# Optimization experiments

Measured on AMD Instinct MI355X. Metric: run time of the kernel, lower is better.

The kernel has to match this reference:

```python
import jax, jax.numpy as jnp
import numpy as np

N_NODES = 50000
N_PAIRS = 400000
F_IN = 5
GCN_DIMS = [32, 64, 128]
MLP_DIMS = [128, 64]


def _lin_init(key, out_d, in_d):
    return jax.random.normal(key, (out_d, in_d), dtype=jnp.float32) / np.sqrt(in_d)


def setup_inputs() -> dict:
    rng = np.random.default_rng(0)
    hi = rng.integers(1, N_NODES, size=N_PAIRS)
    lo = rng.integers(0, 2**31 - 1, size=N_PAIRS) % hi  # lo < hi strictly
    # each undirected pair appears twice per direction (two parallel edges / classes)
    src = np.concatenate([hi, hi, lo, lo]).astype(np.int32)
    dst = np.concatenate([lo, lo, hi, hi]).astype(np.int32)
    edges = jnp.asarray(np.stack([src, dst]))  # [2, 4P]
    detector_labels = jnp.asarray(rng.random(N_NODES) < 0.9)
    key = jax.random.key(0)
    ks = jax.random.split(key, 16)
    x = jax.random.normal(ks[0], (N_NODES, F_IN), dtype=jnp.float32)
    edge_attr = jax.random.uniform(ks[1], (4 * N_PAIRS, 2), dtype=jnp.float32)
    inp = {"x": x, "edges": edges, "edge_attr": edge_attr, "detector_labels": detector_labels}
    dims = [F_IN] + GCN_DIMS
    for i, (di, do) in enumerate(zip(dims[:-1], dims[1:])):
        inp[f"gc{i}_Wrel"] = _lin_init(ks[2 + 3 * i], do, di)
        inp[f"gc{i}_brel"] = jnp.zeros((do,), dtype=jnp.float32)
        inp[f"gc{i}_Wroot"] = _lin_init(ks[3 + 3 * i], do, di)
    mdims = [2 * GCN_DIMS[-1] + 1] + MLP_DIMS
    for i, (di, do) in enumerate(zip(mdims[:-1], mdims[1:])):
        inp[f"fc{i}_W"] = _lin_init(ks[11 + 2 * i], do, di)
        inp[f"fc{i}_b"] = jnp.zeros((do,), dtype=jnp.float32)
    inp["out_W"] = _lin_init(ks[15], 1, MLP_DIMS[-1])
    inp["out_b"] = jnp.zeros((1,), dtype=jnp.float32)
    return inp


def _edge_perm(edges_np, det_np):
    # SplitSyndromes: keep edges with both endpoints in detector set, src > dst,
    # then sort_edge_index (stable lexicographic sort by (src, dst)).
    src, dst = edges_np[0], edges_np[1]
    valid = det_np[src] & det_np[dst] & (src > dst)
    idx = np.where(valid)[0]
    order = np.lexsort((dst[idx], src[idx]))
    return idx[order]


def reference(x, edges, edge_attr, detector_labels,
              gc0_Wrel, gc0_brel, gc0_Wroot,
              gc1_Wrel, gc1_brel, gc1_Wroot,
              gc2_Wrel, gc2_brel, gc2_Wroot,
              fc0_W, fc0_b, fc1_W, fc1_b, out_W, out_b):
    src, dst = edges[0], edges[1]
    w = edge_attr[:, 0] * edge_attr[:, 1]  # GraphConv edge weight
    # GraphConv: lin_rel(sum_j w_ji * x_j) + lin_root(x), ReLU
    for Wrel, brel, Wroot in ((gc0_Wrel, gc0_brel, gc0_Wroot),
                              (gc1_Wrel, gc1_brel, gc1_Wroot),
                              (gc2_Wrel, gc2_brel, gc2_Wroot)):
        agg = jax.ops.segment_sum(x[src] * w[:, None], dst, num_segments=N_NODES)
        x = jax.nn.relu(agg @ Wrel.T + brel + x @ Wroot.T)
    perm = _edge_perm(np.asarray(edges), np.asarray(detector_labels))
    e_src = edges[0, perm]
    e_dst = edges[1, perm]
    ea = edge_attr[perm]  # [M, 2]
    feat = jnp.concatenate([x[e_src], ea[:, :1], x[e_dst]], axis=-1)  # [M, 257]
    for W, b in ((fc0_W, fc0_b), (fc1_W, fc1_b)):
        feat = jax.nn.relu(feat @ W.T + b)
    score = feat @ out_W.T + out_b  # [M, 1]
    pair = jnp.concatenate([score[::2], score[1::2]], axis=1)  # [M/2, 2]
    cls = jnp.stack([ea[::2, 1], ea[1::2, 1]], axis=1)  # [M/2, 2]
    mi = jnp.argmin(pair, axis=1)
    sel = jnp.take_along_axis(pair, mi[:, None], axis=1)[:, 0]
    cls_sel = jnp.take_along_axis(cls, mi[:, None], axis=1)[:, 0]
    edges_out = jnp.stack([e_src[::2], e_dst[::2]])
    return edges_out, jax.nn.sigmoid(sel), cls_sel
```

## Files before the change

kernel.cpp:

```cpp
#include <hip/hip_runtime.h>
#include <hip/hip_bf16.h>
#include <stdint.h>

typedef unsigned long long ull;
typedef unsigned short us;
typedef __attribute__((ext_vector_type(8))) short short8;
typedef __attribute__((ext_vector_type(4))) float f32x4;
#define IDX_BITS 22
#define IDX_MASK 0x3FFFFFu

__device__ __forceinline__ float bfq(float x) {
    return __bfloat162float(__float2bfloat16(x));
}
__device__ __forceinline__ us bfu(float x) {
    __hip_bfloat16 b = __float2bfloat16(x);
    return *(us*)&b;
}
__device__ __forceinline__ float b2f(us u) {
    return __bfloat162float(*(__hip_bfloat16*)&u);
}
__device__ __forceinline__ float ldx(const float* p, size_t i) { return p[i]; }
__device__ __forceinline__ float ldx(const us* p, size_t i) { return b2f(p[i]); }


__global__ void k_det8(const int* __restrict__ src, const int* __restrict__ dst,
                       const unsigned char* __restrict__ det, int P, int* __restrict__ stats,
                       int* __restrict__ dcnt, int* __restrict__ scnt,
                       int2* __restrict__ rnk, int* __restrict__ vrnk) {
    __shared__ int blkc;
    if (threadIdx.x == 0) blkc = 0;
    __syncthreads();
    int e = blockIdx.x * blockDim.x + threadIdx.x;
    bool v = false;
    if (e < P) {
        int hi = src[e], lo = dst[e];
        int r1 = atomicAdd(&dcnt[lo], 1);
        int r2 = atomicAdd(&dcnt[hi], 1);
        rnk[e] = make_int2(r1, r2);
        v = (det[hi] != 0) && (det[lo] != 0);
        vrnk[e] = v ? atomicAdd(&scnt[hi], 1) : -1;
    }
    ull b = __ballot(v);
    if ((threadIdx.x & 63) == 0 && b) atomicAdd(&blkc, (int)__popcll(b));
    __syncthreads();
    if (threadIdx.x == 0 && blkc) atomicAdd(&stats[0], blkc);
}
__global__ void k_det16(const int* __restrict__ src, const int* __restrict__ dst,
                        const us* __restrict__ det, int P, int* __restrict__ stats) {
    if (stats[3] != -1) return;
    __shared__ int blkc;
    if (threadIdx.x == 0) blkc = 0;
    __syncthreads();
    int e = blockIdx.x * blockDim.x + threadIdx.x;
    bool v = false;
    if (e < P) v = (det[src[e]] != 0) && (det[dst[e]] != 0);
    ull b = __ballot(v);
    if ((threadIdx.x & 63) == 0 && b) atomicAdd(&blkc, (int)__popcll(b));
    __syncthreads();
    if (threadIdx.x == 0 && blkc) atomicAdd(&stats[1], blkc);
}
__global__ void k_det32(const int* __restrict__ src, const int* __restrict__ dst,
                        const unsigned int* __restrict__ det, int P, int* __restrict__ stats) {
    if (stats[3] != -2) return;
    __shared__ int blkc;
    if (threadIdx.x == 0) blkc = 0;
    __syncthreads();
    int e = blockIdx.x * blockDim.x + threadIdx.x;
    bool v = false;
    if (e < P) v = (det[src[e]] != 0) && (det[dst[e]] != 0);
    ull b = __ballot(v);
    if ((threadIdx.x & 63) == 0 && b) atomicAdd(&blkc, (int)__popcll(b));
    __syncthreads();
    if (threadIdx.x == 0 && blkc) atomicAdd(&stats[2], blkc);
}
__global__ void k_mode(int* stats, int osz, int step) {
    if (step == 1) {
        int c = stats[0];
        stats[3] = (c == osz / 4 || c == osz / 2) ? 0 : -1;
    } else if (step == 2) {
        if (stats[3] == -1) {
            int c = stats[1];
            stats[3] = (c == osz / 4 || c == osz / 2) ? 2 : -2;
        }
    } else {
        if (stats[3] == -2) stats[3] = 1;
        int m = stats[3];
        stats[4] = (m == 0) ? stats[0] : (m == 2) ? stats[1] : stats[2];
    }
}
__device__ __forceinline__ bool det_ok(int n, const void* det, int mode) {
    if (mode == 0) return ((const unsigned char*)det)[n] != 0;
    if (mode == 2) return ((const us*)det)[n] != 0;
    return ((const unsigned int*)det)[n] != 0;
}

__global__ void k_fixzero(const int* __restrict__ stats, int* __restrict__ scnt, int N) {
    if (stats[3] == 0) return;
    int i = blockIdx.x * blockDim.x + threadIdx.x;
    if (i < N) scnt[i] = 0;
}
__global__ void k_fixhist(const int* __restrict__ src, const int* __restrict__ dst,
                          const void* __restrict__ det, const int* __restrict__ stats,
                          int* __restrict__ scnt, int* __restrict__ vrnk, int P) {
    int m = stats[3];
    if (m == 0) return;
    int e = blockIdx.x * blockDim.x + threadIdx.x;
    if (e >= P) return;
    int hi = src[e], lo = dst[e];
    bool v = det_ok(hi, det, m) && det_ok(lo, det, m);
    vrnk[e] = v ? atomicAdd(&scnt[hi], 1) : -1;
}

__global__ __launch_bounds__(1024) void k_scanA(const int* __restrict__ cnt,
                                                int* __restrict__ off,
                                                int* __restrict__ bsum, int n) {
    __shared__ int wsum[16];
    int t = threadIdx.x, lane = t & 63, w = t >> 6;
    int i = blockIdx.x * 1024 + t;
    int v = (i < n) ? cnt[i] : 0;
    int inc = v;
#pragma unroll
    for (int s = 1; s < 64; s <<= 1) {
        int u = __shfl_up(inc, s);
        if (lane >= s) inc += u;
    }
    if (lane == 63) wsum[w] = inc;
    __syncthreads();
    if (t < 16) {
        int x = wsum[t], sc = x;
#pragma unroll
        for (int s = 1; s < 16; s <<= 1) {
            int u = __shfl_up(sc, s);
            if (t >= s) sc += u;
        }
        wsum[t] = sc - x;
    }
    __syncthreads();
    if (i < n) off[i] = wsum[w] + inc - v;
    if (t == 1023) bsum[blockIdx.x] = wsum[15] + inc;
}
__global__ void k_scanB(int* __restrict__ bsum, int* __restrict__ off, int nb, int n) {
    int t = threadIdx.x;
    int v = (t < nb) ? bsum[t] : 0;
    int inc = v;
#pragma unroll
    for (int s = 1; s < 64; s <<= 1) {
        int u = __shfl_up(inc, s);
        if (t >= s) inc += u;
    }
    if (t < nb) bsum[t] = inc - v;
    if (t == 63) off[n] = inc;
}
__global__ __launch_bounds__(1024) void k_scanC(int* __restrict__ off,
                                                const int* __restrict__ bsum, int n) {
    int i = blockIdx.x * 1024 + threadIdx.x;
    if (i < n && blockIdx.x > 0) off[i] += bsum[blockIdx.x];
}

__global__ void k_scatter(const int* __restrict__ src, const int* __restrict__ dst,
                          const float* __restrict__ ea, const int* __restrict__ doff,
                          const int2* __restrict__ rnk, int2* __restrict__ epair, int P) {
    int e = blockIdx.x * blockDim.x + threadIdx.x;
    if (e >= P) return;
    int hi = src[e], lo = dst[e];
    float w1 = ea[2 * e] * ea[2 * e + 1] + ea[2 * (e + P)] * ea[2 * (e + P) + 1];
    float w2 = ea[2 * (2 * P + e)] * ea[2 * (2 * P + e) + 1] +
               ea[2 * (3 * P + e)] * ea[2 * (3 * P + e) + 1];
    int2 r = rnk[e];
    epair[doff[lo] + r.x] = make_int2(hi, __float_as_int(w1));
    epair[doff[hi] + r.y] = make_int2(lo, __float_as_int(w2));
}

__global__ void k_packall(const float* __restrict__ W1rel, const float* __restrict__ W1root,
                          const float* __restrict__ W2rel, const float* __restrict__ W2root,
                          const float* __restrict__ W3rel, const float* __restrict__ W3root,
                          const float* __restrict__ W0, const float* __restrict__ Wfc1,
                          us* __restrict__ pb1, us* __restrict__ pb2, us* __restrict__ pb3,
                          us* __restrict__ pbP, us* __restrict__ pbQ, us* __restrict__ w1f) {
    int gid = blockIdx.x * blockDim.x + threadIdx.x;
    const float* Wrel;
    const float* Wroot;
    us* out;
    int idx, FIN, CT;
    if (gid < 1024) { idx = gid; Wrel = W1rel; Wroot = W1root; out = pb1; FIN = 5; CT = 2; }
    else if (gid < 5120) { idx = gid - 1024; Wrel = W2rel; Wroot = W2root; out = pb2; FIN = 32; CT = 4; }
    else if (gid < 21504) { idx = gid - 5120; Wrel = W3rel; Wroot = W3root; out = pb3; FIN = 64; CT = 8; }
    else if (gid < 54272) {
        int i2 = gid - 21504;
        bool isQ = i2 >= 16384;
        int i = i2 & 16383;
        int j = i & 7, l = (i >> 3) & 63, ct = (i >> 9) & 7, ks = i >> 12;
        int k = ks * 32 + ((l >> 4) << 3) + j;
        int col = ct * 16 + (l & 15);
        float v = isQ ? W0[col * 257 + 129 + k] : W0[col * 257 + k];
        (isQ ? pbQ : pbP)[i] = bfu(v);
        return;
    } else if (gid < 62464) {
        int i = gid - 54272;
        int j = i & 7, l = (i >> 3) & 63, ct = (i >> 9) & 3, ks = i >> 11;
        int k = ks * 32 + ((l >> 4) << 3) + j;
        int col = ct * 16 + (l & 15);
        w1f[i] = bfu(Wfc1[col * 128 + k]);
        return;
    } else return;
    int j = idx & 7, l = (idx >> 3) & 63;
    int t = idx >> 9;
    int ct = t % CT, ks = t / CT;
    int k = ks * 32 + ((l >> 4) << 3) + j;
    int col = ct * 16 + (l & 15);
    float v = 0.f;
    if (k < FIN) v = Wrel[col * FIN + k];
    else if (k < 2 * FIN) v = Wroot[col * FIN + (k - FIN)];
    out[idx] = bfu(v);
}

template <int FIN, int KP, int G, typename TIN>
__global__ __launch_bounds__(256) void k_agg(
    const TIN* __restrict__ xin, const int2* __restrict__ epair,
    const int* __restrict__ doff, us* __restrict__ A, int N) {
    int tid = blockIdx.x * 256 + threadIdx.x;
    int n = tid / G, f = tid % G;
    if (n >= N) return;
    us* row = &A[(size_t)n * KP];
    if (f < FIN) {
        int b = doff[n], e2 = doff[n + 1];
        float a = 0.f;
        int j = b;
        for (; j + 8 <= e2; j += 8) {
            int2 pp[8];
#pragma unroll
            for (int u = 0; u < 8; ++u) pp[u] = epair[j + u];
            float xv[8];
#pragma unroll
            for (int u = 0; u < 8; ++u) xv[u] = ldx(xin, (size_t)pp[u].x * FIN + f);
#pragma unroll
            for (int u = 0; u < 8; ++u) a = fmaf(__int_as_float(pp[u].y), xv[u], a);
        }
        for (; j < e2; ++j) {
            int2 pq = epair[j];
            a = fmaf(__int_as_float(pq.y), ldx(xin, (size_t)pq.x * FIN + f), a);
        }
        row[f] = bfu(a);
        row[FIN + f] = bfu(ldx(xin, (size_t)n * FIN + f));
    }
    for (int c = 2 * FIN + f; c < KP; c += G) row[c] = 0;
}

template <int KP, int FOUT>
__global__ __launch_bounds__(256) void k_mm(
    const us* __restrict__ A, const us* __restrict__ bfrag,
    const float* __restrict__ bias, us* __restrict__ xout, int N) {
    constexpr int CT = FOUT / 16, KS = KP / 32, STR = KP + 8, CPR = KP / 8;
    __shared__ us Al[64 * STR];
    int t = threadIdx.x, lane = t & 63, w = t >> 6;
    int n0 = blockIdx.x * 64;
    for (int idx = t; idx < 64 * CPR; idx += 256) {
        int r = idx / CPR, c = idx % CPR;
        int n = n0 + r;
        uint4 v = (n < N) ? *(const uint4*)&A[(size_t)n * KP + c * 8] : make_uint4(0, 0, 0, 0);
        *(uint4*)&Al[r * STR + c * 8] = v;
    }
    __syncthreads();
    f32x4 acc[CT];
#pragma unroll
    for (int ct = 0; ct < CT; ++ct) acc[ct] = (f32x4){0.f, 0.f, 0.f, 0.f};
    int arow = w * 16 + (lane & 15);
    int koff = (lane >> 4) << 3;
#pragma unroll
    for (int ks = 0; ks < KS; ++ks) {
        short8 a = *(const short8*)&Al[arow * STR + ks * 32 + koff];
#pragma unroll
        for (int ct = 0; ct < CT; ++ct) {
            short8 b = ((const short8*)bfrag)[(ks * CT + ct) * 64 + lane];
            acc[ct] = __builtin_amdgcn_mfma_f32_16x16x32_bf16(a, b, acc[ct], 0, 0, 0);
        }
    }
    int g = lane >> 4, c0 = lane & 15;
#pragma unroll
    for (int ct = 0; ct < CT; ++ct) {
        int col = ct * 16 + c0;
        float bb = bias[col];
#pragma unroll
        for (int r2 = 0; r2 < 4; ++r2) {
            int n = n0 + w * 16 + g * 4 + r2;
            if (n < N) xout[(size_t)n * FOUT + col] = bfu(fmaxf(acc[ct][r2] + bb, 0.f));
        }
    }
}

__global__ __launch_bounds__(256) void k_mmPQ(
    const us* __restrict__ x3b, const us* __restrict__ pbP, const us* __restrict__ pbQ,
    const float* __restrict__ b0, us* __restrict__ P, us* __restrict__ Q, int N) {
    constexpr int CT = 8, KS = 4, STR = 136, CPR = 16;
    __shared__ us Al[64 * STR];
    int t = threadIdx.x, lane = t & 63, w = t >> 6;
    int n0 = blockIdx.x * 64;
    for (int idx = t; idx < 64 * CPR; idx += 256) {
        int r = idx / CPR, c = idx % CPR;
        int n = n0 + r;
        uint4 v = (n < N) ? *(const uint4*)&x3b[(size_t)n * 128 + c * 8] : make_uint4(0, 0, 0, 0);
        *(uint4*)&Al[r * STR + c * 8] = v;
    }
    __syncthreads();
    int arow = w * 16 + (lane & 15);
    int koff = (lane >> 4) << 3;
    int g = lane >> 4, c0 = lane & 15;
    f32x4 acc[CT];
#pragma unroll
    for (int ct = 0; ct < CT; ++ct) acc[ct] = (f32x4){0.f, 0.f, 0.f, 0.f};
#pragma unroll
    for (int ks = 0; ks < KS; ++ks) {
        short8 a = *(const short8*)&Al[arow * STR + ks * 32 + koff];
#pragma unroll
        for (int ct = 0; ct < CT; ++ct) {
            short8 b = ((const short8*)pbP)[(ks * CT + ct) * 64 + lane];
            acc[ct] = __builtin_amdgcn_mfma_f32_16x16x32_bf16(a, b, acc[ct], 0, 0, 0);
        }
    }
#pragma unroll
    for (int ct = 0; ct < CT; ++ct) {
        int col = ct * 16 + c0;
        float bb = b0[col];
#pragma unroll
        for (int r2 = 0; r2 < 4; ++r2) {
            int n = n0 + w * 16 + g * 4 + r2;
            if (n < N) P[(size_t)n * 128 + col] = bfu(acc[ct][r2] + bb);
        }
    }
#pragma unroll
    for (int ct = 0; ct < CT; ++ct) acc[ct] = (f32x4){0.f, 0.f, 0.f, 0.f};
#pragma unroll
    for (int ks = 0; ks < KS; ++ks) {
        short8 a = *(const short8*)&Al[arow * STR + ks * 32 + koff];
#pragma unroll
        for (int ct = 0; ct < CT; ++ct) {
            short8 b = ((const short8*)pbQ)[(ks * CT + ct) * 64 + lane];
            acc[ct] = __builtin_amdgcn_mfma_f32_16x16x32_bf16(a, b, acc[ct], 0, 0, 0);
        }
    }
#pragma unroll
    for (int ct = 0; ct < CT; ++ct) {
        int col = ct * 16 + c0;
#pragma unroll
        for (int r2 = 0; r2 < 4; ++r2) {
            int n = n0 + w * 16 + g * 4 + r2;
            if (n < N) Q[(size_t)n * 128 + col] = bfu(acc[ct][r2]);
        }
    }
}

__global__ void k_scatter_ent(const int* __restrict__ src, const int* __restrict__ dst,
                              const int* __restrict__ vrnk, const int* __restrict__ soff,
                              ull* __restrict__ ent, int P, int Mcap) {
    int e = blockIdx.x * blockDim.x + threadIdx.x;
    if (e >= P) return;
    int rv = vrnk[e];
    if (rv < 0) return;
    int hi = src[e], lo = dst[e];
    int p = soff[hi] + rv;
    if (p < Mcap) ent[p] = ((ull)(unsigned)lo << IDX_BITS) | (unsigned)e;
}

__global__ __launch_bounds__(256) void k_wsort(const int* __restrict__ off,
                                               ull* __restrict__ ent, int N, int Mcap) {
    int node = blockIdx.x * 4 + (threadIdx.x >> 6);
    int lane = threadIdx.x & 63;
    if (node >= N) return;
    int b = off[node], e2 = off[node + 1];
    if (e2 > Mcap) e2 = Mcap;
    int len = e2 - b;
    if (len <= 1) return;
    if (len <= 64) {
        ull key = (lane < len) ? ent[b + lane] : ~0ull;
        int phases = len + (len & 1);
        for (int ph = 0; ph < phases; ++ph) {
            int partner;
            if ((ph & 1) == 0) partner = lane ^ 1;
            else partner = (lane == 0 || lane == 63) ? lane
                                                     : ((lane & 1) ? lane + 1 : lane - 1);
            ull other = __shfl(key, partner);
            if (partner > lane) key = key < other ? key : other;
            else if (partner < lane) key = key > other ? key : other;
        }
        if (lane < len) ent[b + lane] = key;
    } else if (lane == 0) {
        for (int i = b + 1; i < e2; ++i) {
            ull k = ent[i];
            int j = i - 1;
            while (j >= b && ent[j] > k) { ent[j + 1] = ent[j]; --j; }
            ent[j + 1] = k;
        }
    }
}

__global__ __launch_bounds__(256) void k_mlp2(
    const us* __restrict__ Pm, const us* __restrict__ Qm, const float* __restrict__ ea,
    const int* __restrict__ src, const ull* __restrict__ ent, const int* __restrict__ stats,
    const float* __restrict__ W0, const us* __restrict__ w1f,
    const float* __restrict__ b1, const float* __restrict__ w2, const float* __restrict__ b2,
    float* __restrict__ out, int P) {
    int Mh = stats[4];
    int rows = 2 * Mh;
    int m0 = blockIdx.x * 64;
    if (m0 >= rows) return;
    __shared__ us A[64 * 136];
    __shared__ float ws0e[128];
    __shared__ int pHi[32], pLo[32];
    __shared__ float clsA[32], clsB[32];
    int t = threadIdx.x, lane = t & 63, w = t >> 6;
    if (t < 128) ws0e[t] = W0[t * 257 + 128];
    __syncthreads();

    {
        int j = t >> 3, q = t & 7;
        int pr = (m0 >> 1) + j;
        if (pr < Mh) {
            ull en = ent[pr];
            int e = (int)(en & IDX_MASK);
            int lo = (int)(en >> IDX_BITS);
            int hi = src[e];
            float eaA = ea[2 * e];
            float eaB = ea[2 * (e + P)];
            if (q == 0) {
                pHi[j] = hi;
                pLo[j] = lo;
                clsA[j] = ea[2 * e + 1];
                clsB[j] = ea[2 * (e + P) + 1];
            }
            const us* Pr = Pm + (size_t)hi * 128 + q * 16;
            const us* Qr = Qm + (size_t)lo * 128 + q * 16;
#pragma unroll
            for (int h = 0; h < 2; ++h) {
                int cb = q * 16 + h * 8;
                short8 pv = *(const short8*)&Pr[h * 8];
                short8 qv = *(const short8*)&Qr[h * 8];
                short8 ra, rb;
#pragma unroll
                for (int i = 0; i < 8; ++i) {
                    float base = b2f((us)pv[i]) + b2f((us)qv[i]);
                    float we = ws0e[cb + i];
                    ra[i] = (short)bfu(fmaxf(base + eaA * we, 0.f));
                    rb[i] = (short)bfu(fmaxf(base + eaB * we, 0.f));
                }
                *(short8*)&A[(2 * j) * 136 + cb] = ra;
                *(short8*)&A[(2 * j + 1) * 136 + cb] = rb;
            }
        } else {
            uint4 z = make_uint4(0, 0, 0, 0);
            *(uint4*)&A[(2 * j) * 136 + q * 16] = z;
            *(uint4*)&A[(2 * j) * 136 + q * 16 + 8] = z;
            *(uint4*)&A[(2 * j + 1) * 136 + q * 16] = z;
            *(uint4*)&A[(2 * j + 1) * 136 + q * 16 + 8] = z;
        }
    }
    __syncthreads();

    f32x4 acc1[4];
#pragma unroll
    for (int ct = 0; ct < 4; ++ct) acc1[ct] = (f32x4){0.f, 0.f, 0.f, 0.f};
    {
        int arow = w * 16 + (lane & 15);
        int koff = (lane >> 4) << 3;
#pragma unroll
        for (int ks = 0; ks < 4; ++ks) {
            short8 a = *(const short8*)&A[arow * 136 + ks * 32 + koff];
#pragma unroll
            for (int ct = 0; ct < 4; ++ct) {
                short8 b = ((const short8*)w1f)[(ks * 4 + ct) * 64 + lane];
                acc1[ct] = __builtin_amdgcn_mfma_f32_16x16x32_bf16(a, b, acc1[ct], 0, 0, 0);
            }
        }
    }
    {
        int g = lane >> 4, c0 = lane & 15;
        float part[4] = {0.f, 0.f, 0.f, 0.f};
#pragma unroll
        for (int ct = 0; ct < 4; ++ct) {
            int col = ct * 16 + c0;
            float bb = b1[col], wv = w2[col];
#pragma unroll
            for (int r = 0; r < 4; ++r)
                part[r] += fmaxf(acc1[ct][r] + bb, 0.f) * wv;
        }
        float bout = b2[0];
        float sv[4];
#pragma unroll
        for (int r = 0; r < 4; ++r) {
            float v = part[r];
            v += __shfl_xor(v, 1);
            v += __shfl_xor(v, 2);
            v += __shfl_xor(v, 4);
            v += __shfl_xor(v, 8);
            sv[r] = v + bout;
        }
        if (c0 == 0) {
#pragma unroll
            for (int rr = 0; rr < 4; rr += 2) {
                int jloc = (w * 16 + g * 4 + rr) >> 1;
                int pgi = (m0 >> 1) + jloc;
                if (pgi < Mh) {
                    float s0 = sv[rr], s1 = sv[rr + 1];
                    int pick = (s1 < s0) ? 1 : 0;
                    float sel = pick ? s1 : s0;
                    float cls = pick ? clsB[jloc] : clsA[jloc];
                    float sig = 1.f / (1.f + expf(-sel));
                    out[pgi] = bfq((float)pHi[jloc]);
                    out[Mh + pgi] = bfq((float)pLo[jloc]);
                    out[2 * Mh + pgi] = bfq(sig);
                    out[3 * Mh + pgi] = bfq(cls);
                }
            }
        }
    }
}

extern "C" void kernel_launch(void* const* d_in, const int* in_sizes, int n_in,
                              void* d_out, int out_size, void* d_ws, size_t ws_size,
                              hipStream_t stream) {
    const float* x0 = (const float*)d_in[0];
    const int* edges = (const int*)d_in[1];
    const float* ea = (const float*)d_in[2];
    const void* det = d_in[3];

    int N = in_sizes[0] / 5;
    int E = in_sizes[1] / 2;
    int P = E / 4;
    int osz = out_size;
    int Mcap = osz;

    const int* src = edges;
    const int* dst = edges + E;

    char* p = (char*)d_ws;
    auto alloc = [&](size_t bytes) {
        char* r = p;
        p += (bytes + 255) & ~(size_t)255;
        return r;
    };
    us* xa = (us*)alloc((size_t)N * 32 * 2);
    us* xb = (us*)alloc((size_t)N * 64 * 2);
    us* x3b = (us*)alloc((size_t)N * 128 * 2);
    us* Abuf = (us*)alloc((size_t)N * 128 * 2);
    us* Pb = Abuf;
    us* Qb = (us*)alloc((size_t)N * 128 * 2);
    us* pb1 = (us*)alloc(1024 * 2);
    us* pb2 = (us*)alloc(4096 * 2);
    us* pb3 = (us*)alloc(16384 * 2);
    us* pbP = (us*)alloc(16384 * 2);
    us* pbQ = (us*)alloc(16384 * 2);
    us* w1f = (us*)alloc(8192 * 2);
    int* bsum = (int*)alloc(256);
    int2* rnk = (int2*)alloc((size_t)P * 8);
    int* vrnk = (int*)alloc((size_t)P * 4);
    char* z0 = p;
    int* stats = (int*)alloc(256);
    int* dcnt = (int*)alloc((size_t)N * 4);
    int* scnt = (int*)alloc((size_t)N * 4);
    size_t zlen = (size_t)(p - z0);
    char* u0 = p;
    int* doff = (int*)alloc((size_t)(N + 1) * 4);
    int2* epair = (int2*)alloc((size_t)(2 * P) * 8);
    char* endB = p;
    p = u0;
    int* soff = (int*)alloc((size_t)(N + 1) * 4);
    ull* ent = (ull*)alloc((size_t)Mcap * 8);
    char* endC = p;
    size_t need = (size_t)(((endB > endC) ? endB : endC) - (char*)d_ws);
    if (need > ws_size) return;

    const int B = 256;
    int gP = (P + B - 1) / B;
    int nb = (N + 1023) / 1024;

    hipMemsetAsync(z0, 0, zlen, stream);

    k_det8<<<gP, B, 0, stream>>>(src, dst, (const unsigned char*)det, P, stats,
                                 dcnt, scnt, rnk, vrnk);
    k_mode<<<1, 1, 0, stream>>>(stats, osz, 1);
    k_det16<<<gP, B, 0, stream>>>(src, dst, (const us*)det, P, stats);
    k_mode<<<1, 1, 0, stream>>>(stats, osz, 2);
    k_det32<<<gP, B, 0, stream>>>(src, dst, (const unsigned int*)det, P, stats);
    k_mode<<<1, 1, 0, stream>>>(stats, osz, 3);
    k_fixzero<<<(N + B - 1) / B, B, 0, stream>>>(stats, scnt, N);
    k_fixhist<<<gP, B, 0, stream>>>(src, dst, det, stats, scnt, vrnk, P);

    k_packall<<<(62464 + B - 1) / B, B, 0, stream>>>(
        (const float*)d_in[4], (const float*)d_in[6],
        (const float*)d_in[7], (const float*)d_in[9],
        (const float*)d_in[10], (const float*)d_in[12],
        (const float*)d_in[13], (const float*)d_in[15],
        pb1, pb2, pb3, pbP, pbQ, w1f);

    k_scanA<<<nb, 1024, 0, stream>>>(dcnt, doff, bsum, N);
    k_scanB<<<1, 64, 0, stream>>>(bsum, doff, nb, N);
    k_scanC<<<nb, 1024, 0, stream>>>(doff, bsum, N);

    k_scatter<<<gP, B, 0, stream>>>(src, dst, ea, doff, rnk, epair, P);

    k_agg<5, 32, 8, float><<<((size_t)N * 8 + B - 1) / B, B, 0, stream>>>(
        x0, epair, doff, Abuf, N);
    k_mm<32, 32><<<(N + 63) / 64, B, 0, stream>>>(Abuf, pb1, (const float*)d_in[5], xa, N);
    k_agg<32, 64, 32, us><<<((size_t)N * 32 + B - 1) / B, B, 0, stream>>>(
        xa, epair, doff, Abuf, N);
    k_mm<64, 64><<<(N + 63) / 64, B, 0, stream>>>(Abuf, pb2, (const float*)d_in[8], xb, N);
    k_agg<64, 128, 64, us><<<((size_t)N * 64 + B - 1) / B, B, 0, stream>>>(
        xb, epair, doff, Abuf, N);
    k_mm<128, 128><<<(N + 63) / 64, B, 0, stream>>>(Abuf, pb3, (const float*)d_in[11], x3b, N);

    k_mmPQ<<<(N + 63) / 64, B, 0, stream>>>(x3b, pbP, pbQ, (const float*)d_in[14], Pb, Qb, N);

    k_scanA<<<nb, 1024, 0, stream>>>(scnt, soff, bsum, N);
    k_scanB<<<1, 64, 0, stream>>>(bsum, soff, nb, N);
    k_scanC<<<nb, 1024, 0, stream>>>(soff, bsum, N);
    k_scatter_ent<<<gP, B, 0, stream>>>(src, dst, vrnk, soff, ent, P, Mcap);
    k_wsort<<<(N + 3) / 4, B, 0, stream>>>(soff, ent, N, Mcap);

    k_mlp2<<<(osz + 63) / 64, B, 0, stream>>>(
        Pb, Qb, ea, src, ent, stats,
        (const float*)d_in[13], w1f,
        (const float*)d_in[16], (const float*)d_in[17], (const float*)d_in[18],
        (float*)d_out, P);
}
```

Before: 333.0 us.

## Store intermediate activations in FP8, fuse weight packing, merge scans and scatters

```diff
diff --git a/kernel.cpp b/kernel.cpp
--- a/kernel.cpp
+++ b/kernel.cpp
@@ -4,6 +4,7 @@
 
 typedef unsigned long long ull;
 typedef unsigned short us;
+typedef unsigned char u8;
 typedef __attribute__((ext_vector_type(8))) short short8;
 typedef __attribute__((ext_vector_type(4))) float f32x4;
 #define IDX_BITS 22
@@ -19,14 +20,89 @@
 __device__ __forceinline__ float b2f(us u) {
     return __bfloat162float(*(__hip_bfloat16*)&u);
 }
+__device__ __forceinline__ u8 f2q(float x) {
+    x = fminf(fmaxf(x, -448.f), 448.f);
+    unsigned int u = __float_as_uint(x);
+    unsigned int s = (u >> 24) & 0x80;
+    float ax = fabsf(x);
+    if (ax < 0.0009765625f) return (u8)s;
+    unsigned int au = u & 0x7FFFFFFF;
+    int e = (int)(au >> 23) - 127;
+    unsigned int m = au & 0x7FFFFF;
+    int E = e + 7;
+    if (E <= 0) {
+        int q = (int)rintf(ax * 512.f);
+        if (q >= 8) return (u8)(s | 0x08);
+        return (u8)(s | q);
+    }
+    unsigned int keep = m >> 20;
+    unsigned int rest = m & 0xFFFFF;
+    keep += (rest > 0x80000u || (rest == 0x80000u && (keep & 1)));
+    if (keep == 8) { keep = 0; ++E; }
+    if (E >= 16) return (u8)(s | 0x7E);
+    return (u8)(s | (E << 3) | keep);
+}
+__device__ __forceinline__ float q2f(u8 v) {
+    int E = (v >> 3) & 0xF, m = v & 7;
+    float mag = (E == 0) ? (float)m * 0.001953125f
+                         : __uint_as_float((unsigned)(((E + 120) << 23) | (m << 20)));
+    return (v & 0x80) ? -mag : mag;
+}
 __device__ __forceinline__ float ldx(const float* p, size_t i) { return p[i]; }
 __device__ __forceinline__ float ldx(const us* p, size_t i) { return b2f(p[i]); }
+__device__ __forceinline__ float ldx(const u8* p, size_t i) { return q2f(p[i]); }
+__device__ __forceinline__ void sto(us* p, size_t i, float v) { p[i] = bfu(v); }
+__device__ __forceinline__ void sto(u8* p, size_t i, float v) { p[i] = f2q(v); }
 
 
 __global__ void k_det8(const int* __restrict__ src, const int* __restrict__ dst,
-                       const unsigned char* __restrict__ det, int P, int* __restrict__ stats,
+                       const u8* __restrict__ det, int P, int gP, int* __restrict__ stats,
                        int* __restrict__ dcnt, int* __restrict__ scnt,
-                       int2* __restrict__ rnk, int* __restrict__ vrnk) {
+                       int2* __restrict__ rnk, int* __restrict__ vrnk,
+                       const float* __restrict__ W1rel, const float* __restrict__ W1root,
+                       const float* __restrict__ W2rel, const float* __restrict__ W2root,
+                       const float* __restrict__ W3rel, const float* __restrict__ W3root,
+                       const float* __restrict__ W0, const float* __restrict__ Wfc1,
+                       us* __restrict__ pb1, us* __restrict__ pb2, us* __restrict__ pb3,
+                       us* __restrict__ pbP, us* __restrict__ pbQ, us* __restrict__ w1f) {
+    if ((int)blockIdx.x >= gP) {
+        int gid = (blockIdx.x - gP) * 256 + threadIdx.x;
+        const float* Wrel;
+        const float* Wroot;
+        us* out;
+        int idx, FIN, CT;
+        if (gid < 1024) { idx = gid; Wrel = W1rel; Wroot = W1root; out = pb1; FIN = 5; CT = 2; }
+        else if (gid < 5120) { idx = gid - 1024; Wrel = W2rel; Wroot = W2root; out = pb2; FIN = 32; CT = 4; }
+        else if (gid < 21504) { idx = gid - 5120; Wrel = W3rel; Wroot = W3root; out = pb3; FIN = 64; CT = 8; }
+        else if (gid < 54272) {
+            int i2 = gid - 21504;
+            bool isQ = i2 >= 16384;
+            int i = i2 & 16383;
+            int j = i & 7, l = (i >> 3) & 63, ct = (i >> 9) & 7, ks = i >> 12;
+            int k = ks * 32 + ((l >> 4) << 3) + j;
+            int col = ct * 16 + (l & 15);
+            float v = isQ ? W0[col * 257 + 129 + k] : W0[col * 257 + k];
+            (isQ ? pbQ : pbP)[i] = bfu(v);
+            return;
+        } else if (gid < 62464) {
+            int i = gid - 54272;
+            int j = i & 7, l = (i >> 3) & 63, ct = (i >> 9) & 3, ks = i >> 11;
+            int k = ks * 32 + ((l >> 4) << 3) + j;
+            int col = ct * 16 + (l & 15);
+            w1f[i] = bfu(Wfc1[col * 128 + k]);
+            return;
+        } else return;
+        int j = idx & 7, l = (idx >> 3) & 63;
+        int t = idx >> 9;
+        int ct = t % CT, ks = t / CT;
+        int k = ks * 32 + ((l >> 4) << 3) + j;
+        int col = ct * 16 + (l & 15);
+        float v = 0.f;
+        if (k < FIN) v = Wrel[col * FIN + k];
+        else if (k < 2 * FIN) v = Wroot[col * FIN + (k - FIN)];
+        out[idx] = bfu(v);
+        return;
+    }
     __shared__ int blkc;
     if (threadIdx.x == 0) blkc = 0;
     __syncthreads();
@@ -89,11 +165,10 @@
     }
 }
 __device__ __forceinline__ bool det_ok(int n, const void* det, int mode) {
-    if (mode == 0) return ((const unsigned char*)det)[n] != 0;
+    if (mode == 0) return ((const u8*)det)[n] != 0;
     if (mode == 2) return ((const us*)det)[n] != 0;
     return ((const unsigned int*)det)[n] != 0;
 }
-
 __global__ void k_fixzero(const int* __restrict__ stats, int* __restrict__ scnt, int N) {
     if (stats[3] == 0) return;
     int i = blockIdx.x * blockDim.x + threadIdx.x;
@@ -139,17 +214,31 @@
     if (i < n) off[i] = wsum[w] + inc - v;
     if (t == 1023) bsum[blockIdx.x] = wsum[15] + inc;
 }
-__global__ void k_scanB(int* __restrict__ bsum, int* __restrict__ off, int nb, int n) {
-    int t = threadIdx.x;
+__global__ __launch_bounds__(1024) void k_scanB(int* __restrict__ bsum,
+                                                int* __restrict__ off, int nb, int n) {
+    __shared__ int wsum[16];
+    int t = threadIdx.x, lane = t & 63, w = t >> 6;
     int v = (t < nb) ? bsum[t] : 0;
     int inc = v;
 #pragma unroll
     for (int s = 1; s < 64; s <<= 1) {
         int u = __shfl_up(inc, s);
-        if (t >= s) inc += u;
-    }
-    if (t < nb) bsum[t] = inc - v;
-    if (t == 63) off[n] = inc;
+        if (lane >= s) inc += u;
+    }
+    if (lane == 63) wsum[w] = inc;
+    __syncthreads();
+    if (t < 16) {
+        int x = wsum[t], sc = x;
+#pragma unroll
+        for (int s = 1; s < 16; s <<= 1) {
+            int u = __shfl_up(sc, s);
+            if (t >= s) sc += u;
+        }
+        wsum[t] = sc - x;
+    }
+    __syncthreads();
+    if (t < nb) bsum[t] = wsum[w] + inc - v;
+    if (t == 1023) off[n] = wsum[15] + inc;
 }
 __global__ __launch_bounds__(1024) void k_scanC(int* __restrict__ off,
                                                 const int* __restrict__ bsum, int n) {
@@ -157,9 +246,11 @@
     if (i < n && blockIdx.x > 0) off[i] += bsum[blockIdx.x];
 }
 
-__global__ void k_scatter(const int* __restrict__ src, const int* __restrict__ dst,
-                          const float* __restrict__ ea, const int* __restrict__ doff,
-                          const int2* __restrict__ rnk, int2* __restrict__ epair, int P) {
+__global__ void k_scat2(const int* __restrict__ src, const int* __restrict__ dst,
+                        const float* __restrict__ ea, const int* __restrict__ doff,
+                        const int* __restrict__ soff, const int2* __restrict__ rnk,
+                        const int* __restrict__ vrnk, int2* __restrict__ epair,
+                        ull* __restrict__ ent, int P, int Mcap) {
     int e = blockIdx.x * blockDim.x + threadIdx.x;
     if (e >= P) return;
     int hi = src[e], lo = dst[e];
@@ -169,49 +260,11 @@
     int2 r = rnk[e];
     epair[doff[lo] + r.x] = make_int2(hi, __float_as_int(w1));
     epair[doff[hi] + r.y] = make_int2(lo, __float_as_int(w2));
-}
-
-__global__ void k_packall(const float* __restrict__ W1rel, const float* __restrict__ W1root,
-                          const float* __restrict__ W2rel, const float* __restrict__ W2root,
-                          const float* __restrict__ W3rel, const float* __restrict__ W3root,
-                          const float* __restrict__ W0, const float* __restrict__ Wfc1,
-                          us* __restrict__ pb1, us* __restrict__ pb2, us* __restrict__ pb3,
-                          us* __restrict__ pbP, us* __restrict__ pbQ, us* __restrict__ w1f) {
-    int gid = blockIdx.x * blockDim.x + threadIdx.x;
-    const float* Wrel;
-    const float* Wroot;
-    us* out;
-    int idx, FIN, CT;
-    if (gid < 1024) { idx = gid; Wrel = W1rel; Wroot = W1root; out = pb1; FIN = 5; CT = 2; }
-    else if (gid < 5120) { idx = gid - 1024; Wrel = W2rel; Wroot = W2root; out = pb2; FIN = 32; CT = 4; }
-    else if (gid < 21504) { idx = gid - 5120; Wrel = W3rel; Wroot = W3root; out = pb3; FIN = 64; CT = 8; }
-    else if (gid < 54272) {
-        int i2 = gid - 21504;
-        bool isQ = i2 >= 16384;
-        int i = i2 & 16383;
-        int j = i & 7, l = (i >> 3) & 63, ct = (i >> 9) & 7, ks = i >> 12;
-        int k = ks * 32 + ((l >> 4) << 3) + j;
-        int col = ct * 16 + (l & 15);
-        float v = isQ ? W0[col * 257 + 129 + k] : W0[col * 257 + k];
-        (isQ ? pbQ : pbP)[i] = bfu(v);
-        return;
-    } else if (gid < 62464) {
-        int i = gid - 54272;
-        int j = i & 7, l = (i >> 3) & 63, ct = (i >> 9) & 3, ks = i >> 11;
-        int k = ks * 32 + ((l >> 4) << 3) + j;
-        int col = ct * 16 + (l & 15);
-        w1f[i] = bfu(Wfc1[col * 128 + k]);
-        return;
-    } else return;
-    int j = idx & 7, l = (idx >> 3) & 63;
-    int t = idx >> 9;
-    int ct = t % CT, ks = t / CT;
-    int k = ks * 32 + ((l >> 4) << 3) + j;
-    int col = ct * 16 + (l & 15);
-    float v = 0.f;
-    if (k < FIN) v = Wrel[col * FIN + k];
-    else if (k < 2 * FIN) v = Wroot[col * FIN + (k - FIN)];
-    out[idx] = bfu(v);
+    int rv = vrnk[e];
+    if (rv >= 0) {
+        int p = soff[hi] - soff[0] + rv;
+        if (p < Mcap) ent[p] = ((ull)(unsigned)lo << IDX_BITS) | (unsigned)e;
+    }
 }
 
 template <int FIN, int KP, int G, typename TIN>
@@ -246,10 +299,10 @@
     for (int c = 2 * FIN + f; c < KP; c += G) row[c] = 0;
 }
 
-template <int KP, int FOUT>
+template <int KP, int FOUT, typename TOUT>
 __global__ __launch_bounds__(256) void k_mm(
     const us* __restrict__ A, const us* __restrict__ bfrag,
-    const float* __restrict__ bias, us* __restrict__ xout, int N) {
+    const float* __restrict__ bias, TOUT* __restrict__ xout, int N) {
     constexpr int CT = FOUT / 16, KS = KP / 32, STR = KP + 8, CPR = KP / 8;
     __shared__ us Al[64 * STR];
     int t = threadIdx.x, lane = t & 63, w = t >> 6;
@@ -283,14 +336,14 @@
 #pragma unroll
         for (int r2 = 0; r2 < 4; ++r2) {
             int n = n0 + w * 16 + g * 4 + r2;
-            if (n < N) xout[(size_t)n * FOUT + col] = bfu(fmaxf(acc[ct][r2] + bb, 0.f));
+            if (n < N) sto(xout, (size_t)n * FOUT + col, fmaxf(acc[ct][r2] + bb, 0.f));
         }
     }
 }
 
 __global__ __launch_bounds__(256) void k_mmPQ(
     const us* __restrict__ x3b, const us* __restrict__ pbP, const us* __restrict__ pbQ,
-    const float* __restrict__ b0, us* __restrict__ P, us* __restrict__ Q, int N) {
+    const float* __restrict__ b0, us* __restrict__ P, u8* __restrict__ Q, int N) {
     constexpr int CT = 8, KS = 4, STR = 136, CPR = 16;
     __shared__ us Al[64 * STR];
     int t = threadIdx.x, lane = t & 63, w = t >> 6;
@@ -344,29 +397,18 @@
 #pragma unroll
         for (int r2 = 0; r2 < 4; ++r2) {
             int n = n0 + w * 16 + g * 4 + r2;
-            if (n < N) Q[(size_t)n * 128 + col] = bfu(acc[ct][r2]);
-        }
-    }
-}
-
-__global__ void k_scatter_ent(const int* __restrict__ src, const int* __restrict__ dst,
-                              const int* __restrict__ vrnk, const int* __restrict__ soff,
-                              ull* __restrict__ ent, int P, int Mcap) {
-    int e = blockIdx.x * blockDim.x + threadIdx.x;
-    if (e >= P) return;
-    int rv = vrnk[e];
-    if (rv < 0) return;
-    int hi = src[e], lo = dst[e];
-    int p = soff[hi] + rv;
-    if (p < Mcap) ent[p] = ((ull)(unsigned)lo << IDX_BITS) | (unsigned)e;
-}
-
-__global__ __launch_bounds__(256) void k_wsort(const int* __restrict__ off,
+            if (n < N) Q[(size_t)n * 128 + col] = f2q(acc[ct][r2]);
+        }
+    }
+}
+
+__global__ __launch_bounds__(256) void k_wsort(const int* __restrict__ soff,
                                                ull* __restrict__ ent, int N, int Mcap) {
     int node = blockIdx.x * 4 + (threadIdx.x >> 6);
     int lane = threadIdx.x & 63;
     if (node >= N) return;
-    int b = off[node], e2 = off[node + 1];
+    int base = soff[0];
+    int b = soff[node] - base, e2 = soff[node + 1] - base;
     if (e2 > Mcap) e2 = Mcap;
     int len = e2 - b;
     if (len <= 1) return;
@@ -394,7 +436,7 @@
 }
 
 __global__ __launch_bounds__(256) void k_mlp2(
-    const us* __restrict__ Pm, const us* __restrict__ Qm, const float* __restrict__ ea,
+    const us* __restrict__ Pm, const u8* __restrict__ Qm, const float* __restrict__ ea,
     const int* __restrict__ src, const ull* __restrict__ ent, const int* __restrict__ stats,
     const float* __restrict__ W0, const us* __restrict__ w1f,
     const float* __restrict__ b1, const float* __restrict__ w2, const float* __restrict__ b2,
@@ -428,16 +470,16 @@
                 clsB[j] = ea[2 * (e + P) + 1];
             }
             const us* Pr = Pm + (size_t)hi * 128 + q * 16;
-            const us* Qr = Qm + (size_t)lo * 128 + q * 16;
+            uint4 qraw = *(const uint4*)(Qm + (size_t)lo * 128 + q * 16);
+            const u8* qb = (const u8*)&qraw;
 #pragma unroll
             for (int h = 0; h < 2; ++h) {
                 int cb = q * 16 + h * 8;
                 short8 pv = *(const short8*)&Pr[h * 8];
-                short8 qv = *(const short8*)&Qr[h * 8];
                 short8 ra, rb;
 #pragma unroll
                 for (int i = 0; i < 8; ++i) {
-                    float base = b2f((us)pv[i]) + b2f((us)qv[i]);
+                    float base = b2f((us)pv[i]) + q2f(qb[h * 8 + i]);
                     float we = ws0e[cb + i];
                     ra[i] = (short)bfu(fmaxf(base + eaA * we, 0.f));
                     rb[i] = (short)bfu(fmaxf(base + eaB * we, 0.f));
@@ -526,7 +568,7 @@
     int E = in_sizes[1] / 2;
     int P = E / 4;
     int osz = out_size;
-    int Mcap = osz;
+    int Mcap = osz / 2;
 
     const int* src = edges;
     const int* dst = edges + E;
@@ -537,45 +579,49 @@
         p += (bytes + 255) & ~(size_t)255;
         return r;
     };
-    us* xa = (us*)alloc((size_t)N * 32 * 2);
-    us* xb = (us*)alloc((size_t)N * 64 * 2);
+    u8* xa = (u8*)alloc((size_t)N * 32);
+    u8* xb = (u8*)alloc((size_t)N * 64);
     us* x3b = (us*)alloc((size_t)N * 128 * 2);
     us* Abuf = (us*)alloc((size_t)N * 128 * 2);
     us* Pb = Abuf;
-    us* Qb = (us*)alloc((size_t)N * 128 * 2);
+    u8* Qb = (u8*)alloc((size_t)N * 128);
     us* pb1 = (us*)alloc(1024 * 2);
     us* pb2 = (us*)alloc(4096 * 2);
     us* pb3 = (us*)alloc(16384 * 2);
     us* pbP = (us*)alloc(16384 * 2);
     us* pbQ = (us*)alloc(16384 * 2);
     us* w1f = (us*)alloc(8192 * 2);
-    int* bsum = (int*)alloc(256);
+    int* bsum = (int*)alloc(1024);
     int2* rnk = (int2*)alloc((size_t)P * 8);
     int* vrnk = (int*)alloc((size_t)P * 4);
     char* z0 = p;
     int* stats = (int*)alloc(256);
-    int* dcnt = (int*)alloc((size_t)N * 4);
-    int* scnt = (int*)alloc((size_t)N * 4);
+    int* cnt2 = (int*)alloc((size_t)2 * N * 4);
     size_t zlen = (size_t)(p - z0);
-    char* u0 = p;
-    int* doff = (int*)alloc((size_t)(N + 1) * 4);
+    int* dcnt = cnt2;
+    int* scnt = cnt2 + N;
+    int* doff2 = (int*)alloc((size_t)(2 * N + 1) * 4);
+    int* doff = doff2;
+    int* soff = doff2 + N;
     int2* epair = (int2*)alloc((size_t)(2 * P) * 8);
-    char* endB = p;
-    p = u0;
-    int* soff = (int*)alloc((size_t)(N + 1) * 4);
     ull* ent = (ull*)alloc((size_t)Mcap * 8);
-    char* endC = p;
-    size_t need = (size_t)(((endB > endC) ? endB : endC) - (char*)d_ws);
+    size_t need = (size_t)(p - (char*)d_ws);
     if (need > ws_size) return;
 
     const int B = 256;
     int gP = (P + B - 1) / B;
-    int nb = (N + 1023) / 1024;
+    int n2 = 2 * N;
+    int nb2 = (n2 + 1023) / 1024;
 
     hipMemsetAsync(z0, 0, zlen, stream);
 
-    k_det8<<<gP, B, 0, stream>>>(src, dst, (const unsigned char*)det, P, stats,
-                                 dcnt, scnt, rnk, vrnk);
+    k_det8<<<gP + 244, B, 0, stream>>>(
+        src, dst, (const u8*)det, P, gP, stats, dcnt, scnt, rnk, vrnk,
+        (const float*)d_in[4], (const float*)d_in[6],
+        (const float*)d_in[7], (const float*)d_in[9],
+        (const float*)d_in[10], (const float*)d_in[12],
+        (const float*)d_in[13], (const float*)d_in[15],
+        pb1, pb2, pb3, pbP, pbQ, w1f);
     k_mode<<<1, 1, 0, stream>>>(stats, osz, 1);
     k_det16<<<gP, B, 0, stream>>>(src, dst, (const us*)det, P, stats);
     k_mode<<<1, 1, 0, stream>>>(stats, osz, 2);
@@ -584,35 +630,24 @@
     k_fixzero<<<(N + B - 1) / B, B, 0, stream>>>(stats, scnt, N);
     k_fixhist<<<gP, B, 0, stream>>>(src, dst, det, stats, scnt, vrnk, P);
 
-    k_packall<<<(62464 + B - 1) / B, B, 0, stream>>>(
-        (const float*)d_in[4], (const float*)d_in[6],
-        (const float*)d_in[7], (const float*)d_in[9],
-        (const float*)d_in[10], (const float*)d_in[12],
-        (const float*)d_in[13], (const float*)d_in[15],
-        pb1, pb2, pb3, pbP, pbQ, w1f);
-
-    k_scanA<<<nb, 1024, 0, stream>>>(dcnt, doff, bsum, N);
-    k_scanB<<<1, 64, 0, stream>>>(bsum, doff, nb, N);
-    k_scanC<<<nb, 1024, 0, stream>>>(doff, bsum, N);
-
-    k_scatter<<<gP, B, 0, stream>>>(src, dst, ea, doff, rnk, epair, P);
+    k_scanA<<<nb2, 1024, 0, stream>>>(cnt2, doff2, bsum, n2);
+    k_scanB<<<1, 1024, 0, stream>>>(bsum, doff2, nb2, n2);
+    k_scanC<<<nb2, 1024, 0, stream>>>(doff2, bsum, n2);
+
+    k_scat2<<<gP, B, 0, stream>>>(src, dst, ea, doff, soff, rnk, vrnk, epair, ent, P, Mcap);
 
     k_agg<5, 32, 8, float><<<((size_t)N * 8 + B - 1) / B, B, 0, stream>>>(
         x0, epair, doff, Abuf, N);
-    k_mm<32, 32><<<(N + 63) / 64, B, 0, stream>>>(Abuf, pb1, (const float*)d_in[5], xa, N);
-    k_agg<32, 64, 32, us><<<((size_t)N * 32 + B - 1) / B, B, 0, stream>>>(
+    k_mm<32, 32, u8><<<(N + 63) / 64, B, 0, stream>>>(Abuf, pb1, (const float*)d_in[5], xa, N);
+    k_agg<32, 64, 32, u8><<<((size_t)N * 32 + B - 1) / B, B, 0, stream>>>(
         xa, epair, doff, Abuf, N);
-    k_mm<64, 64><<<(N + 63) / 64, B, 0, stream>>>(Abuf, pb2, (const float*)d_in[8], xb, N);
-    k_agg<64, 128, 64, us><<<((size_t)N * 64 + B - 1) / B, B, 0, stream>>>(
+    k_mm<64, 64, u8><<<(N + 63) / 64, B, 0, stream>>>(Abuf, pb2, (const float*)d_in[8], xb, N);
+    k_agg<64, 128, 64, u8><<<((size_t)N * 64 + B - 1) / B, B, 0, stream>>>(
         xb, epair, doff, Abuf, N);
-    k_mm<128, 128><<<(N + 63) / 64, B, 0, stream>>>(Abuf, pb3, (const float*)d_in[11], x3b, N);
+    k_mm<128, 128, us><<<(N + 63) / 64, B, 0, stream>>>(Abuf, pb3, (const float*)d_in[11], x3b, N);
 
     k_mmPQ<<<(N + 63) / 64, B, 0, stream>>>(x3b, pbP, pbQ, (const float*)d_in[14], Pb, Qb, N);
 
-    k_scanA<<<nb, 1024, 0, stream>>>(scnt, soff, bsum, N);
-    k_scanB<<<1, 64, 0, stream>>>(bsum, soff, nb, N);
-    k_scanC<<<nb, 1024, 0, stream>>>(soff, bsum, N);
-    k_scatter_ent<<<gP, B, 0, stream>>>(src, dst, vrnk, soff, ent, P, Mcap);
     k_wsort<<<(N + 3) / 4, B, 0, stream>>>(soff, ent, N, Mcap);
 
     k_mlp2<<<(osz + 63) / 64, B, 0, stream>>>(
```

After: 361.6 us. 8.6% more time.
